# Kernel optimization log

Measured on AMD Instinct MI355X. Metric: run time of the kernel, lower is better.

Reference implementation:

```python
import jax, jax.numpy as jnp
import numpy as np
import math

# kinematic tree: parent of each of the 23 joints (parents[i] < i -> topological order)
PARENTS = np.array([-1, 0, 1, 1, 3, 4, 5, 4, 7, 4, 9, 1, 11, 12, 13, 12, 15, 12, 17, 0, 19, 0, 21])
NUM_J = 23
HALF, QUART = math.pi / 2.0, math.pi / 4.0
# (joint slot, scale) for the pose params actually written in the torch forward
POSE_SLOTS = [(0, QUART), (3, HALF), (4, HALF), (5, QUART), (7, QUART), (9, QUART),
              (11, HALF), (12, HALF), (13, QUART), (15, QUART), (17, QUART)]


def _rodrigues(r):
    # r: [..., 3] axis-angle -> [..., 3, 3] rotation matrix
    angle = jnp.sqrt(jnp.sum(r * r, axis=-1) + 1e-16)
    axis = r / angle[..., None]
    s, c = jnp.sin(angle), jnp.cos(angle)
    x, y, z = axis[..., 0], axis[..., 1], axis[..., 2]
    zero = jnp.zeros_like(x)
    K = jnp.stack([jnp.stack([zero, -z, y], -1),
                   jnp.stack([z, zero, -x], -1),
                   jnp.stack([-y, x, zero], -1)], -2)
    I = jnp.eye(3, dtype=r.dtype)
    return I + s[..., None, None] * K + (1.0 - c)[..., None, None] * (K @ K)


def _lbs_forward(vertices, joints, weights, displacement, random_dis, pose_params):
    P = displacement.shape[0]
    dt = vertices.dtype
    # per-joint pose: pi/4 or pi/2 * tanh(param) on the used slots, zeros elsewhere
    pose = jnp.zeros((P, NUM_J, 3), dt)
    for (idx, scale), prm in zip(POSE_SLOTS, pose_params):
        pose = pose.at[:, idx].set(scale * jnp.tanh(prm))
    R = _rodrigues(pose)                                          # [P,J,3,3]
    j = joints[0].astype(dt)                                      # [J,3] rest joints
    rel = jnp.concatenate([j[:1], j[1:] - j[PARENTS[1:]]], 0)     # joint offsets from parent
    top = jnp.concatenate([R, jnp.broadcast_to(rel[None, :, :, None], (P, NUM_J, 3, 1))], -1)
    bot = jnp.broadcast_to(jnp.array([0.0, 0.0, 0.0, 1.0], dt), (P, NUM_J, 1, 4))
    T_local = jnp.concatenate([top, bot], -2)                     # [P,J,4,4]
    # forward-kinematics tree walk (fixed 23-joint chain, parents precede children)
    Gs = [T_local[:, 0]]
    for i in range(1, NUM_J):
        Gs.append(Gs[PARENTS[i]] @ T_local[:, i])
    G = jnp.stack(Gs, 1)                                          # [P,J,4,4]
    posed_joints = G[..., :3, 3]                                  # [P,J,3]
    # A = G - [0 | G_rot @ j_rest]  (keep only the 3x4 part actually needed)
    A = G[:, :, :3, :].at[..., 3].add(-jnp.einsum('pjab,jb->pja', G[:, :, :3, :3], j))  # [P,J,3,4]
    W = weights.astype(dt)
    T = jnp.einsum('vj,pjab->pvab', W, A)                         # [P,V,3,4] skinning transforms
    v = vertices[0]                                               # [V,3]
    v_posed = jnp.einsum('pvij,vj->pvi', T[..., :3], v) + T[..., 3]  # [P,V,3]
    shift = random_dis[:, None, :] + 3.0 * jnp.tanh(displacement)   # [P,1,3]
    return v_posed + shift, posed_joints + shift


def setup_inputs():
    P, V, J = 16, 500000, NUM_J
    key = jax.random.key(0)
    ks = jax.random.split(key, 16)
    w = jax.random.uniform(ks[2], (V, J), jnp.float32)
    inp = {
        'vertices': jax.random.normal(ks[0], (1, V, 3), jnp.float32),
        'joints': jax.random.normal(ks[1], (1, J, 3), jnp.float32),
        'weights': w / jnp.sum(w, -1, keepdims=True),  # convex skinning weights
        'displacement': 0.1 * jax.random.normal(ks[3], (P, 1, 3), jnp.float32),
        'random_dis': jax.random.normal(ks[4], (P, 3), jnp.float32),
    }
    names = ['joint_0', 'joint_3', 'joint_4', 'joint_5', 'joint_7', 'joint_9',
             'joint_11', 'joint_12', 'joint_13', 'joint_15', 'joint_17']
    for i, n in enumerate(names):
        inp[n] = jax.random.normal(ks[5 + i], (P, 3), jnp.float32)
    return inp


def reference(vertices, joints, weights, displacement, random_dis, joint_0, joint_3, joint_4, joint_5, joint_7, joint_9, joint_11, joint_12, joint_13, joint_15, joint_17):
    pose_params = (joint_0, joint_3, joint_4, joint_5, joint_7, joint_9,
                   joint_11, joint_12, joint_13, joint_15, joint_17)
    return _lbs_forward(vertices, joints, weights, displacement, random_dis, pose_params)
```

## Files before the change

kernel.cpp:

```cpp
#include <hip/hip_runtime.h>
#include <hip/hip_bf16.h>

typedef __hip_bfloat16 bf16;

#define P_CNT 16
#define J_CNT 23
#define VB    256

struct PosePtrs { const void* p[11]; };

__device__ const int   c_par[J_CNT]  = {-1,0,1,1,3,4,5,4,7,4,9,1,11,12,13,12,15,12,17,0,19,0,21};
__device__ const int   c_slot[J_CNT] = {0,-1,-1,1,2,3,-1,4,-1,5,-1,6,7,8,-1,9,-1,10,-1,-1,-1,-1,-1};
__device__ const float c_scale[11]   = {
    0.7853981633974483f, 1.5707963267948966f, 1.5707963267948966f, 0.7853981633974483f,
    0.7853981633974483f, 0.7853981633974483f, 1.5707963267948966f, 1.5707963267948966f,
    0.7853981633974483f, 0.7853981633974483f, 0.7853981633974483f};

template <bool BF>
__device__ __forceinline__ float ld(const void* p, long long i) {
    if (BF) return __bfloat162float(((const bf16*)p)[i]);
    return ((const float*)p)[i];
}
template <bool BF>
__device__ __forceinline__ void st(void* p, long long i, float v) {
    if (BF) ((bf16*)p)[i] = __float2bfloat16(v);
    else    ((float*)p)[i] = v;
}

template <bool BF>
__device__ __forceinline__ void run(const void* __restrict__ verts,
                                    const void* __restrict__ joints,
                                    const void* __restrict__ weights,
                                    const void* __restrict__ disp,
                                    const void* __restrict__ rdis,
                                    const PosePtrs pp,
                                    void* __restrict__ out, int V,
                                    float* __restrict__ sA,
                                    float* __restrict__ sPose,
                                    float* __restrict__ sSh)
{
    const int t = threadIdx.x;
    const long long vb = (long long)blockIdx.x * VB;

#pragma unroll
    for (int s = 0; s < 11; ++s) {
        if (t < P_CNT * 3) sPose[s * (P_CNT * 3) + t] = ld<BF>(pp.p[s], t);
    }
    if (t < P_CNT) {
#pragma unroll
        for (int cc = 0; cc < 3; ++cc)
            sSh[t * 3 + cc] = ld<BF>(rdis, t * 3 + cc) + 3.f * tanhf(ld<BF>(disp, t * 3 + cc));
    }
    __syncthreads();

#pragma unroll 1
    for (int idx = t; idx < P_CNT * J_CNT; idx += 256) {
        int pq = idx / J_CNT, j = idx - pq * J_CNT;
        float rx = 0.f, ry = 0.f, rz = 0.f;
        int s = c_slot[j];
        if (s >= 0) {
            float sc = c_scale[s];
            rx = sc * tanhf(sPose[s * (P_CNT * 3) + pq * 3 + 0]);
            ry = sc * tanhf(sPose[s * (P_CNT * 3) + pq * 3 + 1]);
            rz = sc * tanhf(sPose[s * (P_CNT * 3) + pq * 3 + 2]);
        }
        float ang = sqrtf(rx * rx + ry * ry + rz * rz + 1e-16f);
        float sn = sinf(ang), cs = cosf(ang);
        float C = 1.f - cs, inva = 1.f / ang;
        float x = rx * inva, y = ry * inva, z = rz * inva;
        float t0 = ld<BF>(joints, j * 3 + 0);
        float t1 = ld<BF>(joints, j * 3 + 1);
        float t2 = ld<BF>(joints, j * 3 + 2);
        if (j != 0) {
            int q = c_par[j];
            t0 -= ld<BF>(joints, q * 3 + 0);
            t1 -= ld<BF>(joints, q * 3 + 1);
            t2 -= ld<BF>(joints, q * 3 + 2);
        }
        float* Ar = sA + idx * 12;
        Ar[0]  = 1.f - C * (y * y + z * z); Ar[1]  = -sn * z + C * x * y;       Ar[2]  = sn * y + C * x * z;        Ar[3]  = t0;
        Ar[4]  = sn * z + C * x * y;        Ar[5]  = 1.f - C * (x * x + z * z); Ar[6]  = -sn * x + C * y * z;       Ar[7]  = t1;
        Ar[8]  = -sn * y + C * x * z;       Ar[9]  = sn * x + C * y * z;        Ar[10] = 1.f - C * (x * x + y * y); Ar[11] = t2;
    }
    __syncthreads();

    if (t < P_CNT) {
        float* Gp = sA + t * (J_CNT * 12);
#pragma unroll 1
        for (int j = 1; j < J_CNT; ++j) {
            const float* Gq = Gp + c_par[j] * 12;
            float* Tj = Gp + j * 12;
            float4 gq0 = *(const float4*)(Gq + 0);
            float4 gq1 = *(const float4*)(Gq + 4);
            float4 gq2 = *(const float4*)(Gq + 8);
            float4 r0 = *(const float4*)(Tj + 0);
            float4 r1 = *(const float4*)(Tj + 4);
            float4 r2 = *(const float4*)(Tj + 8);
            float4 o0, o1, o2;
            o0.x = gq0.x*r0.x + gq0.y*r1.x + gq0.z*r2.x;
            o0.y = gq0.x*r0.y + gq0.y*r1.y + gq0.z*r2.y;
            o0.z = gq0.x*r0.z + gq0.y*r1.z + gq0.z*r2.z;
            o0.w = gq0.x*r0.w + gq0.y*r1.w + gq0.z*r2.w + gq0.w;
            o1.x = gq1.x*r0.x + gq1.y*r1.x + gq1.z*r2.x;
            o1.y = gq1.x*r0.y + gq1.y*r1.y + gq1.z*r2.y;
            o1.z = gq1.x*r0.z + gq1.y*r1.z + gq1.z*r2.z;
            o1.w = gq1.x*r0.w + gq1.y*r1.w + gq1.z*r2.w + gq1.w;
            o2.x = gq2.x*r0.x + gq2.y*r1.x + gq2.z*r2.x;
            o2.y = gq2.x*r0.y + gq2.y*r1.y + gq2.z*r2.y;
            o2.z = gq2.x*r0.z + gq2.y*r1.z + gq2.z*r2.z;
            o2.w = gq2.x*r0.w + gq2.y*r1.w + gq2.z*r2.w + gq2.w;
            *(float4*)(Tj + 0) = o0;
            *(float4*)(Tj + 4) = o1;
            *(float4*)(Tj + 8) = o2;
        }
    }
    __syncthreads();

    {
        const long long pv3 = (long long)P_CNT * V * 3;
#pragma unroll 1
        for (int idx = t; idx < P_CNT * J_CNT; idx += 256) {
            int pq = idx / J_CNT, j = idx - pq * J_CNT;
            float jx = ld<BF>(joints, j * 3 + 0);
            float jy = ld<BF>(joints, j * 3 + 1);
            float jz = ld<BF>(joints, j * 3 + 2);
            float* Ar = sA + idx * 12;
            float g03 = Ar[3], g13 = Ar[7], g23 = Ar[11];
            Ar[3]  = g03 - (Ar[0] * jx + Ar[1] * jy + Ar[2]  * jz);
            Ar[7]  = g13 - (Ar[4] * jx + Ar[5] * jy + Ar[6]  * jz);
            Ar[11] = g23 - (Ar[8] * jx + Ar[9] * jy + Ar[10] * jz);
            if (blockIdx.x == 0) {
                void* out1 = BF ? (void*)((bf16*)out + pv3) : (void*)((float*)out + pv3);
                st<BF>(out1, (long long)idx * 3 + 0, g03 + sSh[pq * 3 + 0]);
                st<BF>(out1, (long long)idx * 3 + 1, g13 + sSh[pq * 3 + 1]);
                st<BF>(out1, (long long)idx * 3 + 2, g23 + sSh[pq * 3 + 2]);
            }
        }
    }
    __syncthreads();

    const long long v = vb + t;
    if (v >= (long long)V) return;

    float w[J_CNT];
    const long long wbase = v * J_CNT;
#pragma unroll
    for (int j = 0; j < J_CNT; ++j) w[j] = ld<BF>(weights, wbase + j);
    float x = ld<BF>(verts, v * 3 + 0);
    float y = ld<BF>(verts, v * 3 + 1);
    float z = ld<BF>(verts, v * 3 + 2);

    const float4* A4 = (const float4*)sA;
    for (int p = 0; p < P_CNT; ++p) {
        const float4* Ap = A4 + p * (J_CNT * 3);
        float4 t0 = make_float4(0.f, 0.f, 0.f, 0.f);
        float4 t1 = make_float4(0.f, 0.f, 0.f, 0.f);
        float4 t2 = make_float4(0.f, 0.f, 0.f, 0.f);
#pragma unroll
        for (int j = 0; j < J_CNT; ++j) {
            float wj = w[j];
            float4 a0 = Ap[j * 3 + 0], a1 = Ap[j * 3 + 1], a2 = Ap[j * 3 + 2];
            t0.x = fmaf(wj, a0.x, t0.x); t0.y = fmaf(wj, a0.y, t0.y);
            t0.z = fmaf(wj, a0.z, t0.z); t0.w = fmaf(wj, a0.w, t0.w);
            t1.x = fmaf(wj, a1.x, t1.x); t1.y = fmaf(wj, a1.y, t1.y);
            t1.z = fmaf(wj, a1.z, t1.z); t1.w = fmaf(wj, a1.w, t1.w);
            t2.x = fmaf(wj, a2.x, t2.x); t2.y = fmaf(wj, a2.y, t2.y);
            t2.z = fmaf(wj, a2.z, t2.z); t2.w = fmaf(wj, a2.w, t2.w);
        }
        float ox = fmaf(t0.x, x, fmaf(t0.y, y, fmaf(t0.z, z, t0.w))) + sSh[p * 3 + 0];
        float oy = fmaf(t1.x, x, fmaf(t1.y, y, fmaf(t1.z, z, t1.w))) + sSh[p * 3 + 1];
        float oz = fmaf(t2.x, x, fmaf(t2.y, y, fmaf(t2.z, z, t2.w))) + sSh[p * 3 + 2];
        long long base = ((long long)p * V + v) * 3;
        st<BF>(out, base + 0, ox);
        st<BF>(out, base + 1, oy);
        st<BF>(out, base + 2, oz);
    }
}

__global__ void __launch_bounds__(256) lbs_all(
    const void* __restrict__ verts,
    const void* __restrict__ joints,
    const void* __restrict__ weights,
    const void* __restrict__ disp,
    const void* __restrict__ rdis,
    PosePtrs pp,
    void* __restrict__ out,
    int V)
{
    __shared__ __align__(16) float sA[P_CNT * J_CNT * 12];
    __shared__ float sPose[11 * P_CNT * 3];
    __shared__ float sSh[P_CNT * 3];
    __shared__ int   sFlag;

    if (threadIdx.x == 0) {
        const float* wf = (const float*)weights;
        const bf16*  wb = (const bf16*)weights;
        bool ok_f = true, ok_b = true;
        for (int r = 0; r < 4; ++r) {
            float sf = 0.f, sb = 0.f;
            for (int j = 0; j < J_CNT; ++j) {
                sf += wf[r * J_CNT + j];
                sb += __bfloat162float(wb[r * J_CNT + j]);
            }
            if (!(fabsf(sf - 1.f) < 0.02f)) ok_f = false;
            if (!(fabsf(sb - 1.f) < 0.10f)) ok_b = false;
        }
        sFlag = (!ok_f && ok_b) ? 1 : 0;
    }
    __syncthreads();
    if (sFlag)
        run<true >(verts, joints, weights, disp, rdis, pp, out, V, sA, sPose, sSh);
    else
        run<false>(verts, joints, weights, disp, rdis, pp, out, V, sA, sPose, sSh);
}

extern "C" void kernel_launch(void* const* d_in, const int* in_sizes, int n_in,
                              void* d_out, int out_size, void* d_ws, size_t ws_size,
                              hipStream_t stream) {
    const void* verts   = d_in[0];
    const void* joints  = d_in[1];
    const void* weights = d_in[2];
    const void* disp    = d_in[3];
    const void* rdis    = d_in[4];
    PosePtrs pp;
    for (int i = 0; i < 11; ++i) pp.p[i] = d_in[5 + i];

    int V = in_sizes[0] / 3;
    int G = (V + VB - 1) / VB;
    lbs_all<<<G, 256, 0, stream>>>(verts, joints, weights, disp, rdis, pp, d_out, V);
}
```

Baseline: 269.3 us.

## Process four vertices per thread with vectorized loads/stores and reordered skinning math

Each thread now handles four consecutive vertices, so one shared-memory read of a per-pose joint matrix is reused across four vertices. Weight, vertex and output accesses use float4 or packed-bf16 vector memory operations instead of scalar ones. The math is reordered so each joint transform is applied to the point before weighting, which removes the blended-matrix accumulation. The cost is more FLOPs per vertex (three dot products per joint per vertex), higher register pressure from 92 weights per thread, and a larger vertex tile (1024 per block), which means fewer blocks and also repeats the per-block joint setup fewer times.

```diff
diff --git a/kernel.cpp b/kernel.cpp
--- a/kernel.cpp
+++ b/kernel.cpp
@@ -5,7 +5,8 @@
 
 #define P_CNT 16
 #define J_CNT 23
-#define VB    256
+#define VPT   4
+#define VB    1024
 
 struct PosePtrs { const void* p[11]; };
 
@@ -25,6 +26,14 @@
 __device__ __forceinline__ void st(void* p, long long i, float v) {
     if (BF) ((bf16*)p)[i] = __float2bfloat16(v);
     else    ((float*)p)[i] = v;
+}
+__device__ __forceinline__ float bflo(unsigned u) { return __uint_as_float(u << 16); }
+__device__ __forceinline__ float bfhi(unsigned u) { return __uint_as_float(u & 0xffff0000u); }
+__device__ __forceinline__ unsigned packbf(float a, float b) {
+    bf16 ha = __float2bfloat16(a), hb = __float2bfloat16(b);
+    unsigned short ua, ub;
+    __builtin_memcpy(&ua, &ha, 2); __builtin_memcpy(&ub, &hb, 2);
+    return ((unsigned)ub << 16) | (unsigned)ua;
 }
 
 template <bool BF>
@@ -139,41 +148,112 @@
     }
     __syncthreads();
 
-    const long long v = vb + t;
-    if (v >= (long long)V) return;
-
-    float w[J_CNT];
-    const long long wbase = v * J_CNT;
-#pragma unroll
-    for (int j = 0; j < J_CNT; ++j) w[j] = ld<BF>(weights, wbase + j);
-    float x = ld<BF>(verts, v * 3 + 0);
-    float y = ld<BF>(verts, v * 3 + 1);
-    float z = ld<BF>(verts, v * 3 + 2);
+    const long long v0 = vb + (long long)t * VPT;
+    if (v0 >= (long long)V) return;
+    const bool full = ((v0 + VPT) <= (long long)V) && ((V & 3) == 0);
+
+    float w[VPT * J_CNT];
+    float px[VPT], py[VPT], pz[VPT];
+
+    if (full) {
+        if (!BF) {
+            const float4* wp = (const float4*)((const float*)weights + v0 * J_CNT);
+#pragma unroll
+            for (int k = 0; k < J_CNT; ++k) {
+                float4 q = wp[k];
+                w[4*k+0] = q.x; w[4*k+1] = q.y; w[4*k+2] = q.z; w[4*k+3] = q.w;
+            }
+            const float4* vp = (const float4*)((const float*)verts + v0 * 3);
+            float4 q0 = vp[0], q1 = vp[1], q2 = vp[2];
+            px[0] = q0.x; py[0] = q0.y; pz[0] = q0.z;
+            px[1] = q0.w; py[1] = q1.x; pz[1] = q1.y;
+            px[2] = q1.z; py[2] = q1.w; pz[2] = q2.x;
+            px[3] = q2.y; py[3] = q2.z; pz[3] = q2.w;
+        } else {
+            const uint2* wp = (const uint2*)((const bf16*)weights + v0 * J_CNT);
+#pragma unroll
+            for (int k = 0; k < J_CNT; ++k) {
+                uint2 u = wp[k];
+                w[4*k+0] = bflo(u.x); w[4*k+1] = bfhi(u.x);
+                w[4*k+2] = bflo(u.y); w[4*k+3] = bfhi(u.y);
+            }
+            const uint2* vp = (const uint2*)((const bf16*)verts + v0 * 3);
+            uint2 u0 = vp[0], u1 = vp[1], u2 = vp[2];
+            px[0] = bflo(u0.x); py[0] = bfhi(u0.x); pz[0] = bflo(u0.y);
+            px[1] = bfhi(u0.y); py[1] = bflo(u1.x); pz[1] = bfhi(u1.x);
+            px[2] = bflo(u1.y); py[2] = bfhi(u1.y); pz[2] = bflo(u2.x);
+            px[3] = bfhi(u2.x); py[3] = bflo(u2.y); pz[3] = bfhi(u2.y);
+        }
+    } else {
+#pragma unroll
+        for (int v = 0; v < VPT; ++v) {
+            bool ok = (v0 + v) < (long long)V;
+            px[v] = ok ? ld<BF>(verts, (v0 + v) * 3 + 0) : 0.f;
+            py[v] = ok ? ld<BF>(verts, (v0 + v) * 3 + 1) : 0.f;
+            pz[v] = ok ? ld<BF>(verts, (v0 + v) * 3 + 2) : 0.f;
+#pragma unroll
+            for (int j = 0; j < J_CNT; ++j)
+                w[v * J_CNT + j] = ok ? ld<BF>(weights, (v0 + v) * J_CNT + j) : 0.f;
+        }
+    }
 
     const float4* A4 = (const float4*)sA;
+#pragma unroll 1
     for (int p = 0; p < P_CNT; ++p) {
         const float4* Ap = A4 + p * (J_CNT * 3);
-        float4 t0 = make_float4(0.f, 0.f, 0.f, 0.f);
-        float4 t1 = make_float4(0.f, 0.f, 0.f, 0.f);
-        float4 t2 = make_float4(0.f, 0.f, 0.f, 0.f);
+        float ox[VPT], oy[VPT], oz[VPT];
+#pragma unroll
+        for (int v = 0; v < VPT; ++v) { ox[v] = 0.f; oy[v] = 0.f; oz[v] = 0.f; }
 #pragma unroll
         for (int j = 0; j < J_CNT; ++j) {
-            float wj = w[j];
             float4 a0 = Ap[j * 3 + 0], a1 = Ap[j * 3 + 1], a2 = Ap[j * 3 + 2];
-            t0.x = fmaf(wj, a0.x, t0.x); t0.y = fmaf(wj, a0.y, t0.y);
-            t0.z = fmaf(wj, a0.z, t0.z); t0.w = fmaf(wj, a0.w, t0.w);
-            t1.x = fmaf(wj, a1.x, t1.x); t1.y = fmaf(wj, a1.y, t1.y);
-            t1.z = fmaf(wj, a1.z, t1.z); t1.w = fmaf(wj, a1.w, t1.w);
-            t2.x = fmaf(wj, a2.x, t2.x); t2.y = fmaf(wj, a2.y, t2.y);
-            t2.z = fmaf(wj, a2.z, t2.z); t2.w = fmaf(wj, a2.w, t2.w);
-        }
-        float ox = fmaf(t0.x, x, fmaf(t0.y, y, fmaf(t0.z, z, t0.w))) + sSh[p * 3 + 0];
-        float oy = fmaf(t1.x, x, fmaf(t1.y, y, fmaf(t1.z, z, t1.w))) + sSh[p * 3 + 1];
-        float oz = fmaf(t2.x, x, fmaf(t2.y, y, fmaf(t2.z, z, t2.w))) + sSh[p * 3 + 2];
-        long long base = ((long long)p * V + v) * 3;
-        st<BF>(out, base + 0, ox);
-        st<BF>(out, base + 1, oy);
-        st<BF>(out, base + 2, oz);
+#pragma unroll
+            for (int v = 0; v < VPT; ++v) {
+                float d0 = fmaf(a0.x, px[v], fmaf(a0.y, py[v], fmaf(a0.z, pz[v], a0.w)));
+                float d1 = fmaf(a1.x, px[v], fmaf(a1.y, py[v], fmaf(a1.z, pz[v], a1.w)));
+                float d2 = fmaf(a2.x, px[v], fmaf(a2.y, py[v], fmaf(a2.z, pz[v], a2.w)));
+                float wv = w[v * J_CNT + j];
+                ox[v] = fmaf(wv, d0, ox[v]);
+                oy[v] = fmaf(wv, d1, oy[v]);
+                oz[v] = fmaf(wv, d2, oz[v]);
+            }
+        }
+        const float shx = sSh[p * 3 + 0], shy = sSh[p * 3 + 1], shz = sSh[p * 3 + 2];
+#pragma unroll
+        for (int v = 0; v < VPT; ++v) { ox[v] += shx; oy[v] += shy; oz[v] += shz; }
+
+        const long long base = ((long long)p * V + v0) * 3;
+        if (!BF) {
+            if (full) {
+                float4* op = (float4*)((float*)out + base);
+                op[0] = make_float4(ox[0], oy[0], oz[0], ox[1]);
+                op[1] = make_float4(oy[1], oz[1], ox[2], oy[2]);
+                op[2] = make_float4(oz[2], ox[3], oy[3], oz[3]);
+            } else {
+#pragma unroll
+                for (int v = 0; v < VPT; ++v)
+                    if (v0 + v < (long long)V) {
+                        ((float*)out)[base + v * 3 + 0] = ox[v];
+                        ((float*)out)[base + v * 3 + 1] = oy[v];
+                        ((float*)out)[base + v * 3 + 2] = oz[v];
+                    }
+            }
+        } else {
+            if (full) {
+                uint2* op = (uint2*)((bf16*)out + base);
+                op[0] = make_uint2(packbf(ox[0], oy[0]), packbf(oz[0], ox[1]));
+                op[1] = make_uint2(packbf(oy[1], oz[1]), packbf(ox[2], oy[2]));
+                op[2] = make_uint2(packbf(oz[2], ox[3]), packbf(oy[3], oz[3]));
+            } else {
+#pragma unroll
+                for (int v = 0; v < VPT; ++v)
+                    if (v0 + v < (long long)V) {
+                        st<BF>(out, base + v * 3 + 0, ox[v]);
+                        st<BF>(out, base + v * 3 + 1, oy[v]);
+                        st<BF>(out, base + v * 3 + 2, oz[v]);
+                    }
+            }
+        }
     }
 }
 
```

Measured after the change: 355.1 us. 31.9% more time.
